# Optimization experiments

Hardware: AMD Instinct MI355X
Metric: run time of the kernel (lower is better)

## Reference

```python
import jax, jax.numpy as jnp
import numpy as np

B, C, H, W = 2, 256, 64, 64
FEAT = 256          # in_channels * expansion_ratio
HEADS = 8
HS = FEAT // HEADS  # 32
OUT = 256


def setup_inputs() -> dict:
    key = jax.random.key(0)
    ks = jax.random.split(key, 12)
    inp = {
        "x": jax.random.normal(ks[0], (B, C, H, W), jnp.float32),
        "mod_multiplier": jax.random.normal(ks[1], (B, FEAT), jnp.float32),
        "mod_bias": jax.random.normal(ks[2], (B, FEAT), jnp.float32),
        # learned parameters (1x1 convs as matrices)
        "w_qkv": jax.random.normal(ks[3], (3 * FEAT, C), jnp.float32) * 0.02,
        "b_qkv": jnp.zeros((3 * FEAT,), jnp.float32),
        "w_proj": jax.random.normal(ks[4], (OUT, FEAT), jnp.float32) * 0.02,
        "pe_q_h": jax.random.normal(ks[5], (1, FEAT, H, 1), jnp.float32) * 0.02,
        "pe_q_w": jax.random.normal(ks[6], (1, FEAT, 1, W), jnp.float32) * 0.02,
        "pe_k_h": jax.random.normal(ks[7], (1, FEAT, H, 1), jnp.float32) * 0.02,
        "pe_k_w": jax.random.normal(ks[8], (1, FEAT, 1, W), jnp.float32) * 0.02,
        "pre_act_bias": jnp.zeros((1, C, 1, 1), jnp.float32),
        "pre_qkv_bias": jnp.zeros((1, C, 1, 1), jnp.float32),
        "pre_proj_bias": jnp.zeros((1, FEAT, 1, 1), jnp.float32),
        "id_scale": jnp.ones((1, OUT, 1, 1), jnp.float32),
    }
    return inp


def reference(x, mod_multiplier, mod_bias, w_qkv, b_qkv, w_proj,
              pe_q_h, pe_q_w, pe_k_h, pe_k_w,
              pre_act_bias, pre_qkv_bias, pre_proj_bias, id_scale):
    b = x.shape[0]
    # pre-activation (Fixup-style biases)
    x_preact = jax.nn.silu(x + pre_act_bias) + pre_qkv_bias
    # 1x1 conv -> QKV: [b, 3F, H, W]
    qkv = jnp.einsum('bchw,oc->bohw', x_preact, w_qkv) + b_qkv[None, :, None, None]
    q, k, v = jnp.split(qkv, 3, axis=1)
    # additive positional embeddings
    q = q + pe_q_h + pe_q_w
    k = k + pe_k_h + pe_k_w
    # FiLM modulation of query
    q = q * mod_multiplier[:, :, None, None] + mod_bias[:, :, None, None]
    # [b, heads, head_size, H*W]
    q = q.reshape(b, HEADS, HS, H * W)
    k = k.reshape(b, HEADS, HS, H * W)
    v = v.reshape(b, HEADS, HS, H * W)
    scale = jnp.asarray(HS ** 0.5, x.dtype)
    logits = jnp.einsum('bhdn,bhdm->bhnm', q, k) / scale
    weights = jax.nn.softmax(logits, axis=-1)
    attn = jnp.einsum('bhnm,bhdm->bhdn', weights, v)
    attn = attn.reshape(b, FEAT, H, W)
    # output projection (1x1 conv, no bias)
    x_res = jnp.einsum('bchw,oc->bohw', attn + pre_proj_bias, w_proj)
    return x * id_scale + x_res
```

## Files before the change

### kernel.cpp

```cpp
#include <hip/hip_runtime.h>
#include <hip/hip_bf16.h>
#include <cstdint>

#define NB   2
#define NC   256
#define NN   4096
#define NH   8
#define HSZ  32
#define NF   256
#define N3F  768

typedef __bf16 bf16x8 __attribute__((ext_vector_type(8)));
typedef __bf16 bf16x4 __attribute__((ext_vector_type(4)));
typedef short  s16x4  __attribute__((ext_vector_type(4)));
typedef float  floatx4 __attribute__((ext_vector_type(4)));

#define QSCALE 0.25506601622184f

__global__ void k_prep(const float* __restrict__ x, const float* __restrict__ pab,
                       const float* __restrict__ pqb, __bf16* __restrict__ y,
                       const float* __restrict__ wqkv, const float* __restrict__ wproj,
                       __bf16* __restrict__ wqb, __bf16* __restrict__ wpb) {
    __shared__ __bf16 ct[32 * 264];
    int bid = blockIdx.x, tid = threadIdx.x;
    if (bid >= 256) {
        int id = (bid - 256) * 1024 + tid * 4;
        const float* src = (id < 196608) ? (wqkv + id) : (wproj + (id - 196608));
        __bf16* dst = (id < 196608) ? (wqb + id) : (wpb + (id - 196608));
        float4 v = *(const float4*)src;
        bf16x4 o;
        o[0] = (__bf16)v.x; o[1] = (__bf16)v.y; o[2] = (__bf16)v.z; o[3] = (__bf16)v.w;
        *(bf16x4*)dst = o;
        return;
    }
    int b = bid >> 7, nt = bid & 127;
    int n0 = nt * 32;
    int cbase = tid >> 3, nc = tid & 7;
#pragma unroll
    for (int q = 0; q < 8; q++) {
        int c = cbase + q * 32;
        const float4 xv = *(const float4*)(x + ((size_t)b * NC + c) * NN + n0 + nc * 4);
        float bias = pab[c], qb = pqb[c];
        float vs[4] = {xv.x, xv.y, xv.z, xv.w};
#pragma unroll
        for (int i = 0; i < 4; i++) {
            float s = vs[i] + bias;
            float r = s / (1.f + __expf(-s)) + qb;
            ct[(nc * 4 + i) * 264 + c] = (__bf16)r;
        }
    }
    __syncthreads();
#pragma unroll
    for (int q = 0; q < 4; q++) {
        int id = tid + q * 256;
        int n = id >> 5, ck = (id & 31) * 8;
        bf16x8 v = *(const bf16x8*)(ct + n * 264 + ck);
        *(bf16x8*)(y + ((size_t)b * NN + n0 + n) * NC + ck) = v;
    }
}

__launch_bounds__(256)
__global__ void k_qkv(const __bf16* __restrict__ y, const __bf16* __restrict__ wb,
                      const float* __restrict__ bqkv,
                      const float* __restrict__ peqh, const float* __restrict__ peqw,
                      const float* __restrict__ pekh, const float* __restrict__ pekw,
                      const float* __restrict__ mm, const float* __restrict__ mb,
                      __bf16* __restrict__ qs, __bf16* __restrict__ kf, __bf16* __restrict__ vf) {
    __shared__ __bf16 smem[4][64 * 40];
    __bf16* ct = &smem[0][0];
    const int nt = blockIdx.x, ot = blockIdx.y, b = blockIdx.z;
    const int tid = threadIdx.x;
    const int wave = tid >> 6, lane = tid & 63, ln = lane & 15, quad = lane >> 4;
    const int wm = (wave & 1) * 32, wn = (wave >> 1) * 32;
    floatx4 acc[2][2];
#pragma unroll
    for (int i = 0; i < 2; i++)
#pragma unroll
        for (int j = 0; j < 2; j++) acc[i][j] = 0.f;
    const __bf16* ysrc = y + ((size_t)b * NN + nt * 64) * NC;
    const __bf16* wsrc = wb + (size_t)ot * 64 * NC;
    const int r0 = tid >> 2, c0 = (tid & 3) * 8;
    bf16x8 ya = *(const bf16x8*)(ysrc + (size_t)r0 * NC + c0);
    bf16x8 wa = *(const bf16x8*)(wsrc + (size_t)r0 * NC + c0);
    for (int ko = 0; ko < 8; ko++) {
        int buf = ko & 1;
        *(bf16x8*)(&smem[buf][r0 * 40 + c0]) = ya;
        *(bf16x8*)(&smem[2 + buf][r0 * 40 + c0]) = wa;
        __syncthreads();
        if (ko < 7) {
            int kc = (ko + 1) * 32;
            ya = *(const bf16x8*)(ysrc + (size_t)r0 * NC + kc + c0);
            wa = *(const bf16x8*)(wsrc + (size_t)r0 * NC + kc + c0);
        }
        bf16x8 af[2], bfr[2];
#pragma unroll
        for (int ii = 0; ii < 2; ii++) af[ii]  = *(const bf16x8*)(&smem[buf][(wm + ii * 16 + ln) * 40 + quad * 8]);
#pragma unroll
        for (int jj = 0; jj < 2; jj++) bfr[jj] = *(const bf16x8*)(&smem[2 + buf][(wn + jj * 16 + ln) * 40 + quad * 8]);
#pragma unroll
        for (int ii = 0; ii < 2; ii++)
#pragma unroll
            for (int jj = 0; jj < 2; jj++)
                acc[ii][jj] = __builtin_amdgcn_mfma_f32_16x16x32_bf16(af[ii], bfr[jj], acc[ii][jj], 0, 0, 0);
    }
    __syncthreads();
    if (ot < 8) {
#pragma unroll
        for (int ii = 0; ii < 2; ii++)
#pragma unroll
            for (int jj = 0; jj < 2; jj++) {
                int o_l = wn + jj * 16 + ln;
                int o_g = ot * 64 + o_l;
                float bq = bqkv[o_g];
#pragma unroll
                for (int r = 0; r < 4; r++) {
                    int n_l = wm + ii * 16 + quad * 4 + r;
                    float val = acc[ii][jj][r] + bq;
                    if (ot < 4) {
                        val += peqh[o_g * 64 + nt] + peqw[o_g * 64 + n_l];
                        val = val * mm[b * NF + o_g] + mb[b * NF + o_g];
                        val *= QSCALE;
                    } else {
                        int c = o_g - 256;
                        val += pekh[c * 64 + nt] + pekw[c * 64 + n_l];
                    }
                    ct[n_l * 72 + o_l] = (__bf16)val;
                }
            }
        __syncthreads();
#pragma unroll
        for (int q = 0; q < 2; q++) {
            int id = tid + q * 256;
            int n_l = id >> 3, oc = (id & 7) * 8;
            bf16x8 v = *(const bf16x8*)(ct + n_l * 72 + oc);
            int n_g = nt * 64 + n_l;
            int o_g = ot * 64 + oc;
            if (ot < 4) {
                int h = o_g >> 5, d = o_g & 31;
                *(bf16x8*)(qs + (((size_t)b * NH + h) * NN + n_g) * HSZ + d) = v;
            } else {
                int c = o_g - 256, h = c >> 5, d0 = c & 31;
                size_t blk = ((size_t)(b * NH + h) * 256 + (n_g >> 4)) * 512;
                *(bf16x8*)(kf + blk + (d0 >> 3) * 128 + (n_g & 15) * 8) = v;
            }
        }
    } else {
#pragma unroll
        for (int ii = 0; ii < 2; ii++)
#pragma unroll
            for (int jj = 0; jj < 2; jj++) {
                int o_l = wn + jj * 16 + ln;
                float bq = bqkv[ot * 64 + o_l];
#pragma unroll
                for (int r = 0; r < 4; r++) {
                    int n_l = wm + ii * 16 + quad * 4 + r;
                    ct[o_l * 72 + n_l] = (__bf16)(acc[ii][jj][r] + bq);
                }
            }
        __syncthreads();
#pragma unroll
        for (int q = 0; q < 4; q++) {
            int id = tid + q * 256;
            int o_l = id >> 4, ng4 = (id & 15) * 4;
            bf16x4 v = *(const bf16x4*)(ct + o_l * 72 + ng4);
            int c = (ot - 8) * 64 + o_l, h = c >> 5, d = c & 31;
            int dj = d >> 4, lnv = d & 15;
            int m_g = nt * 64 + ng4;
            size_t blk = ((size_t)(b * NH + h) * 256 + (m_g >> 4)) * 512;
            *(bf16x4*)(vf + blk + (((m_g >> 2) & 3) * 16 + lnv) * 8 + dj * 4) = v;
        }
    }
}

__launch_bounds__(256)
__global__ void k_attn(const __bf16* __restrict__ qs, const __bf16* __restrict__ kf,
                       const __bf16* __restrict__ vf,
                       __bf16* __restrict__ po, float* __restrict__ pl) {
    __shared__ __bf16 sbuf[2 * 8192];
    int bi = blockIdx.x;
    int xcd = bi & 7, r = bi >> 3;
    int bh = xcd * 2 + (r & 1);
    int r2 = r >> 1;
    int qt = r2 & 31, half = r2 >> 5;
    int tid = threadIdx.x, wave = tid >> 6, lane = tid & 63, ln = lane & 15, quad = lane >> 4;
    int n0 = qt * 128 + wave * 32;
    const __bf16* qbase = qs + (size_t)bh * NN * HSZ;
    const __bf16* kfb = kf + ((size_t)bh * 256 + half * 128) * 512;
    const __bf16* vfb = vf + ((size_t)bh * 256 + half * 128) * 512;
    bf16x8 qa[2];
    qa[0] = *(const bf16x8*)(qbase + (size_t)(n0 + ln) * HSZ + quad * 8);
    qa[1] = *(const bf16x8*)(qbase + (size_t)(n0 + 16 + ln) * HSZ + quad * 8);
    floatx4 o[2][2], o2[2];
    o[0][0] = 0.f; o[0][1] = 0.f; o[1][0] = 0.f; o[1][1] = 0.f;
    o2[0] = 0.f; o2[1] = 0.f;
    floatx4 zf = 0.f;
    s16x4 ones;
    ones[0] = (short)0x3F80; ones[1] = (short)0x3F80;
    ones[2] = (short)0x3F80; ones[3] = (short)0x3F80;
    const int toff = tid * 8;
    const int lo = lane * 8;
    bf16x8 kr0, kr1, vr0, vr1;
    kr0 = *(const bf16x8*)(kfb + toff);
    kr1 = *(const bf16x8*)(kfb + toff + 2048);
    vr0 = *(const bf16x8*)(vfb + toff);
    vr1 = *(const bf16x8*)(vfb + toff + 2048);
    for (int mt = 0; mt < 16; mt++) {
        int bo = (mt & 1) << 13;
        *(bf16x8*)(sbuf + bo + toff) = kr0;
        *(bf16x8*)(sbuf + bo + toff + 2048) = kr1;
        *(bf16x8*)(sbuf + bo + 4096 + toff) = vr0;
        *(bf16x8*)(sbuf + bo + 4096 + toff + 2048) = vr1;
        __syncthreads();
        if (mt < 15) {
            const __bf16* kn = kfb + (mt + 1) * 4096;
            const __bf16* vn = vfb + (mt + 1) * 4096;
            kr0 = *(const bf16x8*)(kn + toff);
            kr1 = *(const bf16x8*)(kn + toff + 2048);
            vr0 = *(const bf16x8*)(vn + toff);
            vr1 = *(const bf16x8*)(vn + toff + 2048);
        }
        const __bf16* kl = sbuf + bo;
        const __bf16* vl = sbuf + bo + 4096;
#pragma unroll
        for (int j = 0; j < 8; j++) {
            bf16x8 kfr = *(const bf16x8*)(kl + j * 512 + lo);
            bf16x8 vfr = *(const bf16x8*)(vl + j * 512 + lo);
            s16x4 vb0, vb1;
            __builtin_memcpy(&vb0, &vfr, 8);
            __builtin_memcpy(&vb1, (const char*)&vfr + 8, 8);
#pragma unroll
            for (int i = 0; i < 2; i++) {
                floatx4 s = __builtin_amdgcn_mfma_f32_16x16x32_bf16(kfr, qa[i], zf, 0, 0, 0);
                bf16x4 p;
#pragma unroll
                for (int rr = 0; rr < 4; rr++)
                    p[rr] = (__bf16)__builtin_amdgcn_exp2f(s[rr]);
                s16x4 pa;
                __builtin_memcpy(&pa, &p, 8);
                o[i][0] = __builtin_amdgcn_mfma_f32_16x16x16bf16_1k(pa, vb0, o[i][0], 0, 0, 0);
                o[i][1] = __builtin_amdgcn_mfma_f32_16x16x16bf16_1k(pa, vb1, o[i][1], 0, 0, 0);
                o2[i]   = __builtin_amdgcn_mfma_f32_16x16x16bf16_1k(pa, ones, o2[i], 0, 0, 0);
            }
        }
    }
    size_t plbase = (size_t)(half * 16 + bh) * NN;
    if (ln == 0)
#pragma unroll
        for (int i = 0; i < 2; i++)
#pragma unroll
            for (int rr = 0; rr < 4; rr++)
                pl[plbase + n0 + i * 16 + quad * 4 + rr] = o2[i][rr];
    __bf16* ct = sbuf;
#pragma unroll
    for (int i = 0; i < 2; i++)
#pragma unroll
        for (int dj = 0; dj < 2; dj++)
#pragma unroll
            for (int rr = 0; rr < 4; rr++)
                ct[(wave * 32 + i * 16 + quad * 4 + rr) * 32 + dj * 16 + ln] = (__bf16)o[i][dj][rr];
    __syncthreads();
    size_t pobase = ((size_t)(half * 16 + bh) * NN + (size_t)qt * 128) * HSZ;
#pragma unroll
    for (int q = 0; q < 2; q++) {
        int id = tid + q * 256;
        int n_l = id >> 2, dc = (id & 3) * 8;
        *(bf16x8*)(po + pobase + n_l * HSZ + dc) = *(const bf16x8*)(ct + n_l * 32 + dc);
    }
}

__launch_bounds__(256)
__global__ void k_proj(const __bf16* __restrict__ po, const float* __restrict__ pl,
                       const __bf16* __restrict__ wpb, const float* __restrict__ ppb,
                       const float* __restrict__ x, const float* __restrict__ idsc,
                       float* __restrict__ out) {
    __shared__ __bf16 at[64 * 264];
    __shared__ __bf16 bt[2][64 * 40];
    __shared__ float linv[8 * 64];
    __shared__ float ppbs[256];
    int nt = blockIdx.x, ot = blockIdx.y, b = blockIdx.z;
    int tid = threadIdx.x, wave = tid >> 6, lane = tid & 63, ln = lane & 15, quad = lane >> 4;
    int wo = (wave & 1) * 32, wn = (wave >> 1) * 32;
#pragma unroll
    for (int q = 0; q < 8; q++) {
        int id = tid + q * 256;
        int row = id >> 5, fc = (id & 31) * 8;
        *(bf16x8*)(at + row * 264 + fc) = *(const bf16x8*)(wpb + (size_t)(ot * 64 + row) * NF + fc);
    }
#pragma unroll
    for (int q = 0; q < 2; q++) {
        int id = tid + q * 256;
        int h = id >> 6, n_l = id & 63;
        size_t base = (size_t)(b * NH + h) * NN + nt * 64 + n_l;
        linv[id] = 1.f / (pl[base] + pl[base + (size_t)16 * NN]);
    }
    ppbs[tid] = ppb[tid];
    __syncthreads();
    floatx4 acc[2][2];
#pragma unroll
    for (int i = 0; i < 2; i++)
#pragma unroll
        for (int j = 0; j < 2; j++) acc[i][j] = 0.f;
    const int n_l = tid >> 2, dh8 = (tid & 3) * 8;
    const size_t hstep = (size_t)NN * HSZ;
    const size_t half_off = (size_t)16 * NN * HSZ;
    size_t prow = ((size_t)b * NH * NN + (size_t)nt * 64 + n_l) * HSZ + dh8;
    bf16x8 p0 = *(const bf16x8*)(po + prow);
    bf16x8 p1 = *(const bf16x8*)(po + prow + half_off);
    for (int ko = 0; ko < 8; ko++) {
        int buf = ko & 1;
        float iv = linv[ko * 64 + n_l];
        bf16x8 c;
#pragma unroll
        for (int e = 0; e < 8; e++)
            c[e] = (__bf16)(((float)p0[e] + (float)p1[e]) * iv + ppbs[ko * 32 + dh8 + e]);
        *(bf16x8*)(&bt[buf][n_l * 40 + dh8]) = c;
        __syncthreads();
        if (ko < 7) {
            size_t pr = prow + (size_t)(ko + 1) * hstep;
            p0 = *(const bf16x8*)(po + pr);
            p1 = *(const bf16x8*)(po + pr + half_off);
        }
        bf16x8 af[2], bfr[2];
#pragma unroll
        for (int oi = 0; oi < 2; oi++) af[oi]  = *(const bf16x8*)(at + (wo + oi * 16 + ln) * 264 + ko * 32 + quad * 8);
#pragma unroll
        for (int nj = 0; nj < 2; nj++) bfr[nj] = *(const bf16x8*)(&bt[buf][(wn + nj * 16 + ln) * 40 + quad * 8]);
#pragma unroll
        for (int oi = 0; oi < 2; oi++)
#pragma unroll
            for (int nj = 0; nj < 2; nj++)
                acc[oi][nj] = __builtin_amdgcn_mfma_f32_16x16x32_bf16(af[oi], bfr[nj], acc[oi][nj], 0, 0, 0);
    }
#pragma unroll
    for (int oi = 0; oi < 2; oi++)
#pragma unroll
        for (int nj = 0; nj < 2; nj++)
#pragma unroll
            for (int r = 0; r < 4; r++) {
                int o_g = ot * 64 + wo + oi * 16 + quad * 4 + r;
                int n_g = nt * 64 + wn + nj * 16 + ln;
                size_t idx = ((size_t)b * NF + o_g) * NN + n_g;
                out[idx] = x[idx] * idsc[o_g] + acc[oi][nj][r];
            }
}

extern "C" void kernel_launch(void* const* d_in, const int* in_sizes, int n_in,
                              void* d_out, int out_size, void* d_ws, size_t ws_size,
                              hipStream_t stream) {
    (void)in_sizes; (void)n_in; (void)out_size; (void)ws_size;
    const float* x    = (const float*)d_in[0];
    const float* mm   = (const float*)d_in[1];
    const float* mb   = (const float*)d_in[2];
    const float* wqkv = (const float*)d_in[3];
    const float* bqkv = (const float*)d_in[4];
    const float* wproj= (const float*)d_in[5];
    const float* peqh = (const float*)d_in[6];
    const float* peqw = (const float*)d_in[7];
    const float* pekh = (const float*)d_in[8];
    const float* pekw = (const float*)d_in[9];
    const float* pab  = (const float*)d_in[10];
    const float* pqb  = (const float*)d_in[11];
    const float* ppb  = (const float*)d_in[12];
    const float* idsc = (const float*)d_in[13];
    float* out = (float*)d_out;

    __bf16* ws = (__bf16*)d_ws;
    const size_t SEG = 2097152;
    __bf16* y    = ws;
    __bf16* qs   = ws + SEG;
    __bf16* kf   = ws + SEG * 2;
    __bf16* vf   = ws + SEG * 3;
    __bf16* po   = ws + SEG * 4;
    float*  pl   = (float*)(ws + SEG * 6);
    __bf16* wqb  = ws + SEG * 6 + 262144;
    __bf16* wpb  = wqb + 196608;

    hipLaunchKernelGGL(k_prep, dim3(512), dim3(256), 0, stream,
                       x, pab, pqb, y, wqkv, wproj, wqb, wpb);
    hipLaunchKernelGGL(k_qkv,  dim3(64, 12, 2), dim3(256), 0, stream,
                       y, wqb, bqkv, peqh, peqw, pekh, pekw, mm, mb, qs, kf, vf);
    hipLaunchKernelGGL(k_attn, dim3(1024), dim3(256), 0, stream, qs, kf, vf, po, pl);
    hipLaunchKernelGGL(k_proj, dim3(64, 4, 2), dim3(256), 0, stream,
                       po, pl, wpb, ppb, x, idsc, out);
}
```

Baseline: 175.0 us.

## Fuse SiLU prep into QKV GEMM, convert weights inline, shrink attention tiles

Removes the separate prep kernel: SiLU pre-activation and bf16 conversion of x and the QKV weights now happen inside the QKV GEMM load path, and the projection kernel converts fp32 weights on load. This drops one launch and the intermediate bf16 activation round trip through memory. The attention kernel is retiled to 64 queries per block, with 16 per wave and 32 key steps of smaller shared buffers, doubling the grid to 2048 blocks and adding an occupancy hint. The trade-off is that each QKV block recomputes SiLU redundantly across the 12 output tiles and does strided fp32 x loads. Attention also gets less Q reuse per K/V tile load.

```diff
diff --git a/kernel.cpp b/kernel.cpp
--- a/kernel.cpp
+++ b/kernel.cpp
@@ -17,50 +17,9 @@
 
 #define QSCALE 0.25506601622184f
 
-__global__ void k_prep(const float* __restrict__ x, const float* __restrict__ pab,
-                       const float* __restrict__ pqb, __bf16* __restrict__ y,
-                       const float* __restrict__ wqkv, const float* __restrict__ wproj,
-                       __bf16* __restrict__ wqb, __bf16* __restrict__ wpb) {
-    __shared__ __bf16 ct[32 * 264];
-    int bid = blockIdx.x, tid = threadIdx.x;
-    if (bid >= 256) {
-        int id = (bid - 256) * 1024 + tid * 4;
-        const float* src = (id < 196608) ? (wqkv + id) : (wproj + (id - 196608));
-        __bf16* dst = (id < 196608) ? (wqb + id) : (wpb + (id - 196608));
-        float4 v = *(const float4*)src;
-        bf16x4 o;
-        o[0] = (__bf16)v.x; o[1] = (__bf16)v.y; o[2] = (__bf16)v.z; o[3] = (__bf16)v.w;
-        *(bf16x4*)dst = o;
-        return;
-    }
-    int b = bid >> 7, nt = bid & 127;
-    int n0 = nt * 32;
-    int cbase = tid >> 3, nc = tid & 7;
-#pragma unroll
-    for (int q = 0; q < 8; q++) {
-        int c = cbase + q * 32;
-        const float4 xv = *(const float4*)(x + ((size_t)b * NC + c) * NN + n0 + nc * 4);
-        float bias = pab[c], qb = pqb[c];
-        float vs[4] = {xv.x, xv.y, xv.z, xv.w};
-#pragma unroll
-        for (int i = 0; i < 4; i++) {
-            float s = vs[i] + bias;
-            float r = s / (1.f + __expf(-s)) + qb;
-            ct[(nc * 4 + i) * 264 + c] = (__bf16)r;
-        }
-    }
-    __syncthreads();
-#pragma unroll
-    for (int q = 0; q < 4; q++) {
-        int id = tid + q * 256;
-        int n = id >> 5, ck = (id & 31) * 8;
-        bf16x8 v = *(const bf16x8*)(ct + n * 264 + ck);
-        *(bf16x8*)(y + ((size_t)b * NN + n0 + n) * NC + ck) = v;
-    }
-}
-
 __launch_bounds__(256)
-__global__ void k_qkv(const __bf16* __restrict__ y, const __bf16* __restrict__ wb,
+__global__ void k_qkv(const float* __restrict__ x, const float* __restrict__ wqkv,
+                      const float* __restrict__ pab, const float* __restrict__ pqb,
                       const float* __restrict__ bqkv,
                       const float* __restrict__ peqh, const float* __restrict__ peqw,
                       const float* __restrict__ pekh, const float* __restrict__ pekw,
@@ -77,26 +36,47 @@
     for (int i = 0; i < 2; i++)
 #pragma unroll
         for (int j = 0; j < 2; j++) acc[i][j] = 0.f;
-    const __bf16* ysrc = y + ((size_t)b * NN + nt * 64) * NC;
-    const __bf16* wsrc = wb + (size_t)ot * 64 * NC;
+    const int cl = tid & 31, ng = tid >> 5;
     const int r0 = tid >> 2, c0 = (tid & 3) * 8;
-    bf16x8 ya = *(const bf16x8*)(ysrc + (size_t)r0 * NC + c0);
-    bf16x8 wa = *(const bf16x8*)(wsrc + (size_t)r0 * NC + c0);
+    const float* xsrc = x + (size_t)b * NC * NN + nt * 64 + ng * 8;
+    const float* wsrc = wqkv + (size_t)(ot * 64 + r0) * NC + c0;
+    float pav = pab[cl], qbv = pqb[cl];
+    float4 xa0 = *(const float4*)(xsrc + (size_t)cl * NN);
+    float4 xa1 = *(const float4*)(xsrc + (size_t)cl * NN + 4);
+    float4 wa0 = *(const float4*)(wsrc);
+    float4 wa1 = *(const float4*)(wsrc + 4);
     for (int ko = 0; ko < 8; ko++) {
-        int buf = ko & 1;
-        *(bf16x8*)(&smem[buf][r0 * 40 + c0]) = ya;
-        *(bf16x8*)(&smem[2 + buf][r0 * 40 + c0]) = wa;
+        int bo = ko & 1;
+        {
+            float xs[8] = {xa0.x, xa0.y, xa0.z, xa0.w, xa1.x, xa1.y, xa1.z, xa1.w};
+#pragma unroll
+            for (int e = 0; e < 8; e++) {
+                float s = xs[e] + pav;
+                float rr = s / (1.f + __expf(-s)) + qbv;
+                smem[bo][(ng * 8 + e) * 40 + cl] = (__bf16)rr;
+            }
+        }
+        {
+            bf16x8 wb;
+            wb[0] = (__bf16)wa0.x; wb[1] = (__bf16)wa0.y; wb[2] = (__bf16)wa0.z; wb[3] = (__bf16)wa0.w;
+            wb[4] = (__bf16)wa1.x; wb[5] = (__bf16)wa1.y; wb[6] = (__bf16)wa1.z; wb[7] = (__bf16)wa1.w;
+            *(bf16x8*)(&smem[2 + bo][r0 * 40 + c0]) = wb;
+        }
         __syncthreads();
         if (ko < 7) {
             int kc = (ko + 1) * 32;
-            ya = *(const bf16x8*)(ysrc + (size_t)r0 * NC + kc + c0);
-            wa = *(const bf16x8*)(wsrc + (size_t)r0 * NC + kc + c0);
+            pav = pab[kc + cl];
+            qbv = pqb[kc + cl];
+            xa0 = *(const float4*)(xsrc + (size_t)(kc + cl) * NN);
+            xa1 = *(const float4*)(xsrc + (size_t)(kc + cl) * NN + 4);
+            wa0 = *(const float4*)(wsrc + kc);
+            wa1 = *(const float4*)(wsrc + kc + 4);
         }
         bf16x8 af[2], bfr[2];
 #pragma unroll
-        for (int ii = 0; ii < 2; ii++) af[ii]  = *(const bf16x8*)(&smem[buf][(wm + ii * 16 + ln) * 40 + quad * 8]);
-#pragma unroll
-        for (int jj = 0; jj < 2; jj++) bfr[jj] = *(const bf16x8*)(&smem[2 + buf][(wn + jj * 16 + ln) * 40 + quad * 8]);
+        for (int ii = 0; ii < 2; ii++) af[ii]  = *(const bf16x8*)(&smem[bo][(wm + ii * 16 + ln) * 40 + quad * 8]);
+#pragma unroll
+        for (int jj = 0; jj < 2; jj++) bfr[jj] = *(const bf16x8*)(&smem[2 + bo][(wn + jj * 16 + ln) * 40 + quad * 8]);
 #pragma unroll
         for (int ii = 0; ii < 2; ii++)
 #pragma unroll
@@ -172,105 +152,84 @@
     }
 }
 
-__launch_bounds__(256)
+__launch_bounds__(256, 8)
 __global__ void k_attn(const __bf16* __restrict__ qs, const __bf16* __restrict__ kf,
                        const __bf16* __restrict__ vf,
                        __bf16* __restrict__ po, float* __restrict__ pl) {
-    __shared__ __bf16 sbuf[2 * 8192];
+    __shared__ __bf16 sbuf[2 * 4096];
     int bi = blockIdx.x;
     int xcd = bi & 7, r = bi >> 3;
     int bh = xcd * 2 + (r & 1);
     int r2 = r >> 1;
-    int qt = r2 & 31, half = r2 >> 5;
+    int qt = r2 & 63, half = r2 >> 6;
     int tid = threadIdx.x, wave = tid >> 6, lane = tid & 63, ln = lane & 15, quad = lane >> 4;
-    int n0 = qt * 128 + wave * 32;
+    int n0 = qt * 64 + wave * 16;
     const __bf16* qbase = qs + (size_t)bh * NN * HSZ;
     const __bf16* kfb = kf + ((size_t)bh * 256 + half * 128) * 512;
     const __bf16* vfb = vf + ((size_t)bh * 256 + half * 128) * 512;
-    bf16x8 qa[2];
-    qa[0] = *(const bf16x8*)(qbase + (size_t)(n0 + ln) * HSZ + quad * 8);
-    qa[1] = *(const bf16x8*)(qbase + (size_t)(n0 + 16 + ln) * HSZ + quad * 8);
-    floatx4 o[2][2], o2[2];
-    o[0][0] = 0.f; o[0][1] = 0.f; o[1][0] = 0.f; o[1][1] = 0.f;
-    o2[0] = 0.f; o2[1] = 0.f;
+    bf16x8 qa = *(const bf16x8*)(qbase + (size_t)(n0 + ln) * HSZ + quad * 8);
+    floatx4 o[2], o2;
+    o[0] = 0.f; o[1] = 0.f; o2 = 0.f;
     floatx4 zf = 0.f;
     s16x4 ones;
     ones[0] = (short)0x3F80; ones[1] = (short)0x3F80;
     ones[2] = (short)0x3F80; ones[3] = (short)0x3F80;
     const int toff = tid * 8;
     const int lo = lane * 8;
-    bf16x8 kr0, kr1, vr0, vr1;
-    kr0 = *(const bf16x8*)(kfb + toff);
-    kr1 = *(const bf16x8*)(kfb + toff + 2048);
-    vr0 = *(const bf16x8*)(vfb + toff);
-    vr1 = *(const bf16x8*)(vfb + toff + 2048);
-    for (int mt = 0; mt < 16; mt++) {
-        int bo = (mt & 1) << 13;
-        *(bf16x8*)(sbuf + bo + toff) = kr0;
-        *(bf16x8*)(sbuf + bo + toff + 2048) = kr1;
-        *(bf16x8*)(sbuf + bo + 4096 + toff) = vr0;
-        *(bf16x8*)(sbuf + bo + 4096 + toff + 2048) = vr1;
-        __syncthreads();
-        if (mt < 15) {
-            const __bf16* kn = kfb + (mt + 1) * 4096;
-            const __bf16* vn = vfb + (mt + 1) * 4096;
-            kr0 = *(const bf16x8*)(kn + toff);
-            kr1 = *(const bf16x8*)(kn + toff + 2048);
-            vr0 = *(const bf16x8*)(vn + toff);
-            vr1 = *(const bf16x8*)(vn + toff + 2048);
+    bf16x8 kr = *(const bf16x8*)(kfb + toff);
+    bf16x8 vr = *(const bf16x8*)(vfb + toff);
+    for (int mt = 0; mt < 32; mt++) {
+        int bo = (mt & 1) << 12;
+        *(bf16x8*)(sbuf + bo + toff) = kr;
+        *(bf16x8*)(sbuf + bo + 2048 + toff) = vr;
+        __syncthreads();
+        if (mt < 31) {
+            kr = *(const bf16x8*)(kfb + (mt + 1) * 2048 + toff);
+            vr = *(const bf16x8*)(vfb + (mt + 1) * 2048 + toff);
         }
         const __bf16* kl = sbuf + bo;
-        const __bf16* vl = sbuf + bo + 4096;
-#pragma unroll
-        for (int j = 0; j < 8; j++) {
+        const __bf16* vl = sbuf + bo + 2048;
+#pragma unroll
+        for (int j = 0; j < 4; j++) {
             bf16x8 kfr = *(const bf16x8*)(kl + j * 512 + lo);
             bf16x8 vfr = *(const bf16x8*)(vl + j * 512 + lo);
             s16x4 vb0, vb1;
             __builtin_memcpy(&vb0, &vfr, 8);
             __builtin_memcpy(&vb1, (const char*)&vfr + 8, 8);
-#pragma unroll
-            for (int i = 0; i < 2; i++) {
-                floatx4 s = __builtin_amdgcn_mfma_f32_16x16x32_bf16(kfr, qa[i], zf, 0, 0, 0);
-                bf16x4 p;
-#pragma unroll
-                for (int rr = 0; rr < 4; rr++)
-                    p[rr] = (__bf16)__builtin_amdgcn_exp2f(s[rr]);
-                s16x4 pa;
-                __builtin_memcpy(&pa, &p, 8);
-                o[i][0] = __builtin_amdgcn_mfma_f32_16x16x16bf16_1k(pa, vb0, o[i][0], 0, 0, 0);
-                o[i][1] = __builtin_amdgcn_mfma_f32_16x16x16bf16_1k(pa, vb1, o[i][1], 0, 0, 0);
-                o2[i]   = __builtin_amdgcn_mfma_f32_16x16x16bf16_1k(pa, ones, o2[i], 0, 0, 0);
-            }
+            floatx4 s = __builtin_amdgcn_mfma_f32_16x16x32_bf16(kfr, qa, zf, 0, 0, 0);
+            bf16x4 p;
+#pragma unroll
+            for (int rr = 0; rr < 4; rr++)
+                p[rr] = (__bf16)__builtin_amdgcn_exp2f(s[rr]);
+            s16x4 pa;
+            __builtin_memcpy(&pa, &p, 8);
+            o[0] = __builtin_amdgcn_mfma_f32_16x16x16bf16_1k(pa, vb0, o[0], 0, 0, 0);
+            o[1] = __builtin_amdgcn_mfma_f32_16x16x16bf16_1k(pa, vb1, o[1], 0, 0, 0);
+            o2   = __builtin_amdgcn_mfma_f32_16x16x16bf16_1k(pa, ones, o2, 0, 0, 0);
         }
     }
     size_t plbase = (size_t)(half * 16 + bh) * NN;
     if (ln == 0)
 #pragma unroll
-        for (int i = 0; i < 2; i++)
-#pragma unroll
-            for (int rr = 0; rr < 4; rr++)
-                pl[plbase + n0 + i * 16 + quad * 4 + rr] = o2[i][rr];
+        for (int rr = 0; rr < 4; rr++)
+            pl[plbase + n0 + quad * 4 + rr] = o2[rr];
     __bf16* ct = sbuf;
 #pragma unroll
-    for (int i = 0; i < 2; i++)
-#pragma unroll
-        for (int dj = 0; dj < 2; dj++)
-#pragma unroll
-            for (int rr = 0; rr < 4; rr++)
-                ct[(wave * 32 + i * 16 + quad * 4 + rr) * 32 + dj * 16 + ln] = (__bf16)o[i][dj][rr];
+    for (int dj = 0; dj < 2; dj++)
+#pragma unroll
+        for (int rr = 0; rr < 4; rr++)
+            ct[(wave * 16 + quad * 4 + rr) * 32 + dj * 16 + ln] = (__bf16)o[dj][rr];
     __syncthreads();
-    size_t pobase = ((size_t)(half * 16 + bh) * NN + (size_t)qt * 128) * HSZ;
-#pragma unroll
-    for (int q = 0; q < 2; q++) {
-        int id = tid + q * 256;
-        int n_l = id >> 2, dc = (id & 3) * 8;
+    size_t pobase = ((size_t)(half * 16 + bh) * NN + (size_t)qt * 64) * HSZ;
+    {
+        int n_l = tid >> 2, dc = (tid & 3) * 8;
         *(bf16x8*)(po + pobase + n_l * HSZ + dc) = *(const bf16x8*)(ct + n_l * 32 + dc);
     }
 }
 
 __launch_bounds__(256)
 __global__ void k_proj(const __bf16* __restrict__ po, const float* __restrict__ pl,
-                       const __bf16* __restrict__ wpb, const float* __restrict__ ppb,
+                       const float* __restrict__ wproj, const float* __restrict__ ppb,
                        const float* __restrict__ x, const float* __restrict__ idsc,
                        float* __restrict__ out) {
     __shared__ __bf16 at[64 * 264];
@@ -284,7 +243,12 @@
     for (int q = 0; q < 8; q++) {
         int id = tid + q * 256;
         int row = id >> 5, fc = (id & 31) * 8;
-        *(bf16x8*)(at + row * 264 + fc) = *(const bf16x8*)(wpb + (size_t)(ot * 64 + row) * NF + fc);
+        float4 w0 = *(const float4*)(wproj + (size_t)(ot * 64 + row) * NF + fc);
+        float4 w1 = *(const float4*)(wproj + (size_t)(ot * 64 + row) * NF + fc + 4);
+        bf16x8 wb;
+        wb[0] = (__bf16)w0.x; wb[1] = (__bf16)w0.y; wb[2] = (__bf16)w0.z; wb[3] = (__bf16)w0.w;
+        wb[4] = (__bf16)w1.x; wb[5] = (__bf16)w1.y; wb[6] = (__bf16)w1.z; wb[7] = (__bf16)w1.w;
+        *(bf16x8*)(at + row * 264 + fc) = wb;
     }
 #pragma unroll
     for (int q = 0; q < 2; q++) {
@@ -366,20 +330,15 @@
 
     __bf16* ws = (__bf16*)d_ws;
     const size_t SEG = 2097152;
-    __bf16* y    = ws;
-    __bf16* qs   = ws + SEG;
-    __bf16* kf   = ws + SEG * 2;
-    __bf16* vf   = ws + SEG * 3;
-    __bf16* po   = ws + SEG * 4;
-    float*  pl   = (float*)(ws + SEG * 6);
-    __bf16* wqb  = ws + SEG * 6 + 262144;
-    __bf16* wpb  = wqb + 196608;
-
-    hipLaunchKernelGGL(k_prep, dim3(512), dim3(256), 0, stream,
-                       x, pab, pqb, y, wqkv, wproj, wqb, wpb);
+    __bf16* qs   = ws;
+    __bf16* kf   = ws + SEG;
+    __bf16* vf   = ws + SEG * 2;
+    __bf16* po   = ws + SEG * 3;
+    float*  pl   = (float*)(ws + SEG * 5);
+
     hipLaunchKernelGGL(k_qkv,  dim3(64, 12, 2), dim3(256), 0, stream,
-                       y, wqb, bqkv, peqh, peqw, pekh, pekw, mm, mb, qs, kf, vf);
-    hipLaunchKernelGGL(k_attn, dim3(1024), dim3(256), 0, stream, qs, kf, vf, po, pl);
+                       x, wqkv, pab, pqb, bqkv, peqh, peqw, pekh, pekw, mm, mb, qs, kf, vf);
+    hipLaunchKernelGGL(k_attn, dim3(2048), dim3(256), 0, stream, qs, kf, vf, po, pl);
     hipLaunchKernelGGL(k_proj, dim3(64, 4, 2), dim3(256), 0, stream,
-                       po, pl, wpb, ppb, x, idsc, out);
+                       po, pl, wproj, ppb, x, idsc, out);
 }
```

After: 177.8 us. About the same (+1.6%).
